# Optimization experiments

Measured on AMD Instinct MI355X. Metric: run time of the kernel, lower is better.

The kernel has to match this reference:

```python
import jax, jax.numpy as jnp
import numpy as np

N_EMBD = 4096
N_LAYERS = 32
LAYER = 3


def _layer_norm(x, w, b, eps=1e-5):
    mu = jnp.mean(x)
    var = jnp.var(x)
    return (x - mu) * jax.lax.rsqrt(var + eps) * w + b


def setup_inputs() -> dict:
    key = jax.random.key(0)
    ks = jax.random.split(key, 12)
    s = np.float32(1.0 / np.sqrt(N_EMBD))  # keep matvec outputs O(1) so exp() stays sane
    return {
        "input": jax.random.normal(ks[0], (N_EMBD,), jnp.float32),
        "state": jax.random.normal(ks[1], (5 * N_LAYERS, N_EMBD), jnp.float32) * 0.1,
        "time_mix_k": jax.random.uniform(ks[2], (N_EMBD,), jnp.float32),
        "time_mix_v": jax.random.uniform(ks[3], (N_EMBD,), jnp.float32),
        "time_mix_r": jax.random.uniform(ks[4], (N_EMBD,), jnp.float32),
        "time_first": jax.random.normal(ks[5], (N_EMBD,), jnp.float32) * 0.5,
        "time_decay": -jnp.abs(jax.random.normal(ks[6], (N_EMBD,), jnp.float32)),
        "kw": jax.random.normal(ks[7], (N_EMBD, N_EMBD), jnp.float32) * s,
        "vw": jax.random.normal(ks[8], (N_EMBD, N_EMBD), jnp.float32) * s,
        "rw": jax.random.normal(ks[9], (N_EMBD, N_EMBD), jnp.float32) * s,
        "ow": jax.random.normal(ks[10], (N_EMBD, N_EMBD), jnp.float32) * s,
        "ln_weight": jnp.ones((N_EMBD,), jnp.float32),
        "ln_bias": jnp.zeros((N_EMBD,), jnp.float32),
        "layer_num": LAYER,
        "n_embd": N_EMBD,
    }


def reference(input, state, time_mix_k, time_mix_v, time_mix_r, time_first,
              time_decay, kw, vw, rw, ow, ln_weight, ln_bias, layer_num, n_embd):
    # FLOAT_MODE == 'fp32' branch of the original module.
    i = int(layer_num)
    x = _layer_norm(input, ln_weight, ln_bias)

    prev = state[5 * i + 1]  # previous token's post-LN x (time shift)
    xk = x * time_mix_k + prev * (1.0 - time_mix_k)
    xv = x * time_mix_v + prev * (1.0 - time_mix_v)
    xr = x * time_mix_r + prev * (1.0 - time_mix_r)

    r = jax.nn.sigmoid(rw @ xr)
    kk = kw @ xk
    vv = vw @ xv

    aa = state[5 * i + 2]
    bb = state[5 * i + 3]
    pp = state[5 * i + 4]  # running log-max for numerical stability

    # WKV output for this token
    ww = time_first + kk
    p = jnp.maximum(pp, ww)
    e1 = jnp.exp(pp - p)
    e2 = jnp.exp(ww - p)
    a = e1 * aa + e2 * vv
    b = e1 * bb + e2

    # state update
    ww2 = pp + time_decay
    p2 = jnp.maximum(ww2, kk)
    e1s = jnp.exp(ww2 - p2)
    e2s = jnp.exp(kk - p2)
    new_aa = e1s * aa + e2s * vv
    new_bb = e1s * bb + e2s

    new_state = (state
                 .at[5 * i + 1].set(x)
                 .at[5 * i + 2].set(new_aa)
                 .at[5 * i + 3].set(new_bb)
                 .at[5 * i + 4].set(p2))

    wkv = a / b
    out = ow @ (r * wkv)
    return (new_state, out)
```

## Files before the change

kernel.cpp:

```cpp
#include <hip/hip_runtime.h>
#include <math.h>

#define NE 4096
#define NROWS_STATE 160

#define WS_XK   0
#define WS_XV   (NE)
#define WS_XR   (2*NE)
#define WS_KK   (3*NE)
#define WS_VV   (4*NE)
#define WS_RR   (5*NE)
#define WS_RWKV (6*NE)

__device__ __forceinline__ float block_reduce_sum(float v, float* sm) {
    #pragma unroll
    for (int off = 32; off > 0; off >>= 1)
        v += __shfl_down(v, off, 64);
    int lane = threadIdx.x & 63;
    int wid  = threadIdx.x >> 6;
    if (lane == 0) sm[wid] = v;
    __syncthreads();
    int nw = blockDim.x >> 6;
    if (wid == 0) {
        v = (lane < nw) ? sm[lane] : 0.0f;
        #pragma unroll
        for (int off = 32; off > 0; off >>= 1)
            v += __shfl_down(v, off, 64);
    }
    return v;
}

__global__ void k_copy_state(const float4* __restrict__ src, float4* __restrict__ dst, int n4) {
    int i = blockIdx.x * blockDim.x + threadIdx.x;
    if (i < n4) dst[i] = src[i];
}

__global__ void __launch_bounds__(512)
k_ln_mix(const float* __restrict__ in, const float* __restrict__ state,
         const float* __restrict__ tmk, const float* __restrict__ tmv,
         const float* __restrict__ tmr, const float* __restrict__ lnw,
         const float* __restrict__ lnb, const int* __restrict__ layer,
         float* __restrict__ out_state, float* __restrict__ ws) {
    __shared__ float sm1[8];
    __shared__ float sm2[8];
    __shared__ float s_mu, s_rstd;
    int t = threadIdx.x;

    float4 v0 = ((const float4*)in)[t * 2 + 0];
    float4 v1 = ((const float4*)in)[t * 2 + 1];
    float sum   = v0.x + v0.y + v0.z + v0.w + v1.x + v1.y + v1.z + v1.w;
    float sumsq = v0.x*v0.x + v0.y*v0.y + v0.z*v0.z + v0.w*v0.w
                + v1.x*v1.x + v1.y*v1.y + v1.z*v1.z + v1.w*v1.w;

    float tot  = block_reduce_sum(sum, sm1);
    __syncthreads();
    float tot2 = block_reduce_sum(sumsq, sm2);
    if (t == 0) {
        float mu  = tot * (1.0f / NE);
        float var = tot2 * (1.0f / NE) - mu * mu;
        s_mu   = mu;
        s_rstd = rsqrtf(var + 1e-5f);
    }
    __syncthreads();

    float mu = s_mu, rstd = s_rstd;
    int li = layer[0];
    const float* prev_row = state + (size_t)(5 * li + 1) * NE;
    float* x_row = out_state + (size_t)(5 * li + 1) * NE;

    #pragma unroll
    for (int j = 0; j < 8; ++j) {
        int idx = t * 8 + j;
        float xin  = in[idx];
        float x    = (xin - mu) * rstd * lnw[idx] + lnb[idx];
        float prev = prev_row[idx];
        float mk = tmk[idx], mv = tmv[idx], mr = tmr[idx];
        ws[WS_XK + idx] = x * mk + prev * (1.0f - mk);
        ws[WS_XV + idx] = x * mv + prev * (1.0f - mv);
        ws[WS_XR + idx] = x * mr + prev * (1.0f - mr);
        x_row[idx] = x;
    }
}

__global__ void __launch_bounds__(256)
k_matvec3(const float* __restrict__ kw, const float* __restrict__ vw,
          const float* __restrict__ rw, const float* __restrict__ ws_in,
          float* __restrict__ ws_out) {
    int bid = blockIdx.x;
    int m   = bid >> 12;
    int row = bid & (NE - 1);
    const float* W = (m == 0) ? kw : (m == 1) ? vw : rw;
    const float4* Wr = (const float4*)(W + (size_t)row * NE);
    const float4* xv = (const float4*)(ws_in + m * NE);

    int t = threadIdx.x;
    float acc = 0.0f;
    #pragma unroll
    for (int j = 0; j < 4; ++j) {
        float4 w4 = Wr[j * 256 + t];
        float4 x4 = xv[j * 256 + t];
        acc += w4.x * x4.x + w4.y * x4.y + w4.z * x4.z + w4.w * x4.w;
    }
    __shared__ float sm[4];
    float r = block_reduce_sum(acc, sm);
    if (t == 0) {
        if (m == 2) r = 1.0f / (1.0f + expf(-r));
        ws_out[m * NE + row] = r;
    }
}

__global__ void k_wkv(const float* __restrict__ state, const float* __restrict__ tf,
                      const float* __restrict__ td, const int* __restrict__ layer,
                      const float* __restrict__ ws, float* __restrict__ out_state,
                      float* __restrict__ rwkv) {
    int idx = blockIdx.x * blockDim.x + threadIdx.x;
    if (idx >= NE) return;
    int li = layer[0];
    float kk = ws[WS_KK + idx];
    float vv = ws[WS_VV + idx];
    float r  = ws[WS_RR + idx];
    float aa = state[(size_t)(5 * li + 2) * NE + idx];
    float bb = state[(size_t)(5 * li + 3) * NE + idx];
    float pp = state[(size_t)(5 * li + 4) * NE + idx];

    float ww = tf[idx] + kk;
    float p  = fmaxf(pp, ww);
    float e1 = expf(pp - p);
    float e2 = expf(ww - p);
    float a  = e1 * aa + e2 * vv;
    float b  = e1 * bb + e2;

    float ww2 = pp + td[idx];
    float p2  = fmaxf(ww2, kk);
    float e1s = expf(ww2 - p2);
    float e2s = expf(kk - p2);
    out_state[(size_t)(5 * li + 2) * NE + idx] = e1s * aa + e2s * vv;
    out_state[(size_t)(5 * li + 3) * NE + idx] = e1s * bb + e2s;
    out_state[(size_t)(5 * li + 4) * NE + idx] = p2;

    rwkv[idx] = r * (a / b);
}

__global__ void __launch_bounds__(256)
k_matvec_ow(const float* __restrict__ ow, const float* __restrict__ rwkv,
            float* __restrict__ out) {
    int row = blockIdx.x;
    const float4* Wr = (const float4*)(ow + (size_t)row * NE);
    const float4* xv = (const float4*)rwkv;
    int t = threadIdx.x;
    float acc = 0.0f;
    #pragma unroll
    for (int j = 0; j < 4; ++j) {
        float4 w4 = Wr[j * 256 + t];
        float4 x4 = xv[j * 256 + t];
        acc += w4.x * x4.x + w4.y * x4.y + w4.z * x4.z + w4.w * x4.w;
    }
    __shared__ float sm[4];
    float r = block_reduce_sum(acc, sm);
    if (t == 0) out[row] = r;
}

extern "C" void kernel_launch(void* const* d_in, const int* in_sizes, int n_in,
                              void* d_out, int out_size, void* d_ws, size_t ws_size,
                              hipStream_t stream) {
    const float* input = (const float*)d_in[0];
    const float* state = (const float*)d_in[1];
    const float* tmk   = (const float*)d_in[2];
    const float* tmv   = (const float*)d_in[3];
    const float* tmr   = (const float*)d_in[4];
    const float* tf    = (const float*)d_in[5];
    const float* td    = (const float*)d_in[6];
    const float* kw    = (const float*)d_in[7];
    const float* vw    = (const float*)d_in[8];
    const float* rw    = (const float*)d_in[9];
    const float* ow    = (const float*)d_in[10];
    const float* lnw   = (const float*)d_in[11];
    const float* lnb   = (const float*)d_in[12];
    const int*   layer = (const int*)d_in[13];

    float* out_state = (float*)d_out;
    float* out_vec   = (float*)d_out + (size_t)NROWS_STATE * NE;
    float* ws        = (float*)d_ws;

    {
        int n4 = NROWS_STATE * NE / 4;
        k_copy_state<<<(n4 + 255) / 256, 256, 0, stream>>>(
            (const float4*)state, (float4*)out_state, n4);
    }
    k_ln_mix<<<1, 512, 0, stream>>>(input, state, tmk, tmv, tmr, lnw, lnb,
                                    layer, out_state, ws);
    k_matvec3<<<3 * NE, 256, 0, stream>>>(kw, vw, rw, ws, ws + WS_KK);
    k_wkv<<<NE / 256, 256, 0, stream>>>(state, tf, td, layer, ws, out_state,
                                        ws + WS_RWKV);
    k_matvec_ow<<<NE, 256, 0, stream>>>(ow, ws + WS_RWKV, out_vec);
}
```

Before: 59.36 us.

## Fuse state copy with layernorm-mix and use one wave per matvec row

Merges the full state copy into the layernorm/mix kernel, using extra blocks that skip the four rows the later kernels overwrite; this removes one launch and some redundant writes. Both matvec kernels now give each 64-lane wave one output row with four independent accumulators, so the shared-memory block reduction and its barrier go away and each thread has more loads in flight. The layernorm part runs as a single 256-thread block that reuses the input values it already loaded. The kernel still reads the full 256 MB of weights, so the main cost is unchanged and only overhead is reduced.

```diff
diff --git a/kernel.cpp b/kernel.cpp
--- a/kernel.cpp
+++ b/kernel.cpp
@@ -12,73 +12,74 @@
 #define WS_RR   (5*NE)
 #define WS_RWKV (6*NE)
 
-__device__ __forceinline__ float block_reduce_sum(float v, float* sm) {
+__device__ __forceinline__ float wave_reduce_sum(float v) {
     #pragma unroll
     for (int off = 32; off > 0; off >>= 1)
         v += __shfl_down(v, off, 64);
-    int lane = threadIdx.x & 63;
-    int wid  = threadIdx.x >> 6;
-    if (lane == 0) sm[wid] = v;
-    __syncthreads();
-    int nw = blockDim.x >> 6;
-    if (wid == 0) {
-        v = (lane < nw) ? sm[lane] : 0.0f;
-        #pragma unroll
-        for (int off = 32; off > 0; off >>= 1)
-            v += __shfl_down(v, off, 64);
-    }
     return v;
 }
 
-__global__ void k_copy_state(const float4* __restrict__ src, float4* __restrict__ dst, int n4) {
-    int i = blockIdx.x * blockDim.x + threadIdx.x;
-    if (i < n4) dst[i] = src[i];
-}
-
-__global__ void __launch_bounds__(512)
-k_ln_mix(const float* __restrict__ in, const float* __restrict__ state,
-         const float* __restrict__ tmk, const float* __restrict__ tmv,
-         const float* __restrict__ tmr, const float* __restrict__ lnw,
-         const float* __restrict__ lnb, const int* __restrict__ layer,
-         float* __restrict__ out_state, float* __restrict__ ws) {
-    __shared__ float sm1[8];
-    __shared__ float sm2[8];
+__global__ void __launch_bounds__(256)
+k_copy_ln_mix(const float* __restrict__ in, const float* __restrict__ state,
+              const float* __restrict__ tmk, const float* __restrict__ tmv,
+              const float* __restrict__ tmr, const float* __restrict__ lnw,
+              const float* __restrict__ lnb, const int* __restrict__ layer,
+              float* __restrict__ out_state, float* __restrict__ ws) {
+    int li = layer[0];
+    if (blockIdx.x != 0) {
+        int i4 = (blockIdx.x - 1) * 256 + threadIdx.x;
+        int row = i4 >> 10;
+        if (row < 5 * li + 1 || row > 5 * li + 4) {
+            ((float4*)out_state)[i4] = ((const float4*)state)[i4];
+        }
+        return;
+    }
+    __shared__ float sm1[4];
+    __shared__ float sm2[4];
     __shared__ float s_mu, s_rstd;
     int t = threadIdx.x;
-
-    float4 v0 = ((const float4*)in)[t * 2 + 0];
-    float4 v1 = ((const float4*)in)[t * 2 + 1];
-    float sum   = v0.x + v0.y + v0.z + v0.w + v1.x + v1.y + v1.z + v1.w;
-    float sumsq = v0.x*v0.x + v0.y*v0.y + v0.z*v0.z + v0.w*v0.w
-                + v1.x*v1.x + v1.y*v1.y + v1.z*v1.z + v1.w*v1.w;
-
-    float tot  = block_reduce_sum(sum, sm1);
+    int lane = t & 63, wid = t >> 6;
+
+    float4 v[4];
+    float sum = 0.0f, sumsq = 0.0f;
+    #pragma unroll
+    for (int j = 0; j < 4; ++j) {
+        v[j] = ((const float4*)in)[t * 4 + j];
+        sum   += v[j].x + v[j].y + v[j].z + v[j].w;
+        sumsq += v[j].x*v[j].x + v[j].y*v[j].y + v[j].z*v[j].z + v[j].w*v[j].w;
+    }
+    float s1 = wave_reduce_sum(sum);
+    float s2 = wave_reduce_sum(sumsq);
+    if (lane == 0) { sm1[wid] = s1; sm2[wid] = s2; }
     __syncthreads();
-    float tot2 = block_reduce_sum(sumsq, sm2);
     if (t == 0) {
+        float tot = sm1[0] + sm1[1] + sm1[2] + sm1[3];
+        float tot2 = sm2[0] + sm2[1] + sm2[2] + sm2[3];
         float mu  = tot * (1.0f / NE);
         float var = tot2 * (1.0f / NE) - mu * mu;
-        s_mu   = mu;
+        s_mu = mu;
         s_rstd = rsqrtf(var + 1e-5f);
     }
     __syncthreads();
-
     float mu = s_mu, rstd = s_rstd;
-    int li = layer[0];
+
     const float* prev_row = state + (size_t)(5 * li + 1) * NE;
     float* x_row = out_state + (size_t)(5 * li + 1) * NE;
 
     #pragma unroll
-    for (int j = 0; j < 8; ++j) {
-        int idx = t * 8 + j;
-        float xin  = in[idx];
-        float x    = (xin - mu) * rstd * lnw[idx] + lnb[idx];
-        float prev = prev_row[idx];
-        float mk = tmk[idx], mv = tmv[idx], mr = tmr[idx];
-        ws[WS_XK + idx] = x * mk + prev * (1.0f - mk);
-        ws[WS_XV + idx] = x * mv + prev * (1.0f - mv);
-        ws[WS_XR + idx] = x * mr + prev * (1.0f - mr);
-        x_row[idx] = x;
+    for (int j = 0; j < 4; ++j) {
+        #pragma unroll
+        for (int c = 0; c < 4; ++c) {
+            int idx = t * 16 + j * 4 + c;
+            float xin = (c == 0) ? v[j].x : (c == 1) ? v[j].y : (c == 2) ? v[j].z : v[j].w;
+            float x    = (xin - mu) * rstd * lnw[idx] + lnb[idx];
+            float prev = prev_row[idx];
+            float mk = tmk[idx], mv = tmv[idx], mr = tmr[idx];
+            ws[WS_XK + idx] = x * mk + prev * (1.0f - mk);
+            ws[WS_XV + idx] = x * mv + prev * (1.0f - mv);
+            ws[WS_XR + idx] = x * mr + prev * (1.0f - mr);
+            x_row[idx] = x;
+        }
     }
 }
 
@@ -86,26 +87,35 @@
 k_matvec3(const float* __restrict__ kw, const float* __restrict__ vw,
           const float* __restrict__ rw, const float* __restrict__ ws_in,
           float* __restrict__ ws_out) {
-    int bid = blockIdx.x;
-    int m   = bid >> 12;
-    int row = bid & (NE - 1);
+    int lane = threadIdx.x & 63;
+    int gw   = blockIdx.x * 4 + (threadIdx.x >> 6);
+    int m    = gw >> 12;
+    int row  = gw & (NE - 1);
     const float* W = (m == 0) ? kw : (m == 1) ? vw : rw;
     const float4* Wr = (const float4*)(W + (size_t)row * NE);
     const float4* xv = (const float4*)(ws_in + m * NE);
 
-    int t = threadIdx.x;
-    float acc = 0.0f;
-    #pragma unroll
-    for (int j = 0; j < 4; ++j) {
-        float4 w4 = Wr[j * 256 + t];
-        float4 x4 = xv[j * 256 + t];
-        acc += w4.x * x4.x + w4.y * x4.y + w4.z * x4.z + w4.w * x4.w;
-    }
-    __shared__ float sm[4];
-    float r = block_reduce_sum(acc, sm);
-    if (t == 0) {
-        if (m == 2) r = 1.0f / (1.0f + expf(-r));
-        ws_out[m * NE + row] = r;
+    float acc0 = 0.0f, acc1 = 0.0f, acc2 = 0.0f, acc3 = 0.0f;
+    #pragma unroll
+    for (int j = 0; j < 4; ++j) {
+        float4 w0 = Wr[(j*4+0) * 64 + lane];
+        float4 w1 = Wr[(j*4+1) * 64 + lane];
+        float4 w2 = Wr[(j*4+2) * 64 + lane];
+        float4 w3 = Wr[(j*4+3) * 64 + lane];
+        float4 x0 = xv[(j*4+0) * 64 + lane];
+        float4 x1 = xv[(j*4+1) * 64 + lane];
+        float4 x2 = xv[(j*4+2) * 64 + lane];
+        float4 x3 = xv[(j*4+3) * 64 + lane];
+        acc0 += w0.x*x0.x + w0.y*x0.y + w0.z*x0.z + w0.w*x0.w;
+        acc1 += w1.x*x1.x + w1.y*x1.y + w1.z*x1.z + w1.w*x1.w;
+        acc2 += w2.x*x2.x + w2.y*x2.y + w2.z*x2.z + w2.w*x2.w;
+        acc3 += w3.x*x3.x + w3.y*x3.y + w3.z*x3.z + w3.w*x3.w;
+    }
+    float a = (acc0 + acc1) + (acc2 + acc3);
+    a = wave_reduce_sum(a);
+    if (lane == 0) {
+        if (m == 2) a = 1.0f / (1.0f + expf(-a));
+        ws_out[m * NE + row] = a;
     }
 }
 
@@ -144,20 +154,30 @@
 __global__ void __launch_bounds__(256)
 k_matvec_ow(const float* __restrict__ ow, const float* __restrict__ rwkv,
             float* __restrict__ out) {
-    int row = blockIdx.x;
+    int lane = threadIdx.x & 63;
+    int row  = blockIdx.x * 4 + (threadIdx.x >> 6);
     const float4* Wr = (const float4*)(ow + (size_t)row * NE);
     const float4* xv = (const float4*)rwkv;
-    int t = threadIdx.x;
-    float acc = 0.0f;
-    #pragma unroll
-    for (int j = 0; j < 4; ++j) {
-        float4 w4 = Wr[j * 256 + t];
-        float4 x4 = xv[j * 256 + t];
-        acc += w4.x * x4.x + w4.y * x4.y + w4.z * x4.z + w4.w * x4.w;
-    }
-    __shared__ float sm[4];
-    float r = block_reduce_sum(acc, sm);
-    if (t == 0) out[row] = r;
+
+    float acc0 = 0.0f, acc1 = 0.0f, acc2 = 0.0f, acc3 = 0.0f;
+    #pragma unroll
+    for (int j = 0; j < 4; ++j) {
+        float4 w0 = Wr[(j*4+0) * 64 + lane];
+        float4 w1 = Wr[(j*4+1) * 64 + lane];
+        float4 w2 = Wr[(j*4+2) * 64 + lane];
+        float4 w3 = Wr[(j*4+3) * 64 + lane];
+        float4 x0 = xv[(j*4+0) * 64 + lane];
+        float4 x1 = xv[(j*4+1) * 64 + lane];
+        float4 x2 = xv[(j*4+2) * 64 + lane];
+        float4 x3 = xv[(j*4+3) * 64 + lane];
+        acc0 += w0.x*x0.x + w0.y*x0.y + w0.z*x0.z + w0.w*x0.w;
+        acc1 += w1.x*x1.x + w1.y*x1.y + w1.z*x1.z + w1.w*x1.w;
+        acc2 += w2.x*x2.x + w2.y*x2.y + w2.z*x2.z + w2.w*x2.w;
+        acc3 += w3.x*x3.x + w3.y*x3.y + w3.z*x3.z + w3.w*x3.w;
+    }
+    float a = (acc0 + acc1) + (acc2 + acc3);
+    a = wave_reduce_sum(a);
+    if (lane == 0) out[row] = a;
 }
 
 extern "C" void kernel_launch(void* const* d_in, const int* in_sizes, int n_in,
@@ -182,15 +202,10 @@
     float* out_vec   = (float*)d_out + (size_t)NROWS_STATE * NE;
     float* ws        = (float*)d_ws;
 
-    {
-        int n4 = NROWS_STATE * NE / 4;
-        k_copy_state<<<(n4 + 255) / 256, 256, 0, stream>>>(
-            (const float4*)state, (float4*)out_state, n4);
-    }
-    k_ln_mix<<<1, 512, 0, stream>>>(input, state, tmk, tmv, tmr, lnw, lnb,
-                                    layer, out_state, ws);
-    k_matvec3<<<3 * NE, 256, 0, stream>>>(kw, vw, rw, ws, ws + WS_KK);
+    k_copy_ln_mix<<<641, 256, 0, stream>>>(input, state, tmk, tmv, tmr, lnw, lnb,
+                                           layer, out_state, ws);
+    k_matvec3<<<3 * NE / 4, 256, 0, stream>>>(kw, vw, rw, ws, ws + WS_KK);
     k_wkv<<<NE / 256, 256, 0, stream>>>(state, tf, td, layer, ws, out_state,
                                         ws + WS_RWKV);
-    k_matvec_ow<<<NE, 256, 0, stream>>>(ow, ws + WS_RWKV, out_vec);
-}
+    k_matvec_ow<<<NE / 4, 256, 0, stream>>>(ow, ws + WS_RWKV, out_vec);
+}
```

Measured after the change: 58.46 us. No clear change (-1.5%).
